# Optimization experiments

Hardware: AMD Instinct MI355X
Metric: run time of the kernel (lower is better)

## Reference

```python
import jax, jax.numpy as jnp
import numpy as np

N = 10000        # num nodes
E = 160000       # num edges
C = 128          # hidden_channels
SCALE = 0.0625   # scale_factor = 1/avg_degree
EPS = 1.1920929e-07  # torch RMSNorm default eps = finfo(float32).eps


def setup_inputs() -> dict:
    key = jax.random.key(0)
    ks = jax.random.split(key, 10)
    s = jax.random.normal(ks[0], (N, 1, C), dtype=jnp.float32)
    v = jax.random.normal(ks[1], (N, 3, C), dtype=jnp.float32)
    edge_index = jax.random.randint(ks[2], (2, E), 0, N, dtype=jnp.int64)
    rbf_filter = jax.random.normal(ks[3], (E, 1, 3 * C), dtype=jnp.float32)
    edge_vector = jax.random.normal(ks[4], (E, 3), dtype=jnp.float32)
    # phi MLP params (Linear(C,C) -> SiLU -> Dropout(eval) -> Linear(C,3C))
    w1 = jax.random.normal(ks[5], (C, C), dtype=jnp.float32) / np.sqrt(C)
    b1 = jnp.zeros((C,), dtype=jnp.float32)
    w2 = jax.random.normal(ks[6], (3 * C, C), dtype=jnp.float32) / np.sqrt(C)
    b2 = jnp.zeros((3 * C,), dtype=jnp.float32)
    rms_w = jnp.ones((C,), dtype=jnp.float32)  # RMSNorm elementwise affine weight
    return {"s": s, "v": v, "edge_index": edge_index, "rbf_filter": rbf_filter,
            "edge_vector": edge_vector, "w1": w1, "b1": b1, "w2": w2, "b2": b2,
            "rms_w": rms_w}


def reference(s, v, edge_index, rbf_filter, edge_vector, w1, b1, w2, b2, rms_w):
    i, j = edge_index[0], edge_index[1]
    # RMSNorm over last dim
    s_norm = s * jax.lax.rsqrt(jnp.mean(s * s, axis=-1, keepdims=True) + EPS) * rms_w
    # phi MLP (dropout is identity in eval mode)
    h = jax.nn.silu(jnp.einsum('nkc,dc->nkd', s_norm, w1) + b1)
    phi_s = jnp.einsum('nkc,dc->nkd', h, w2) + b2          # [N,1,3C]
    filt = phi_s[j] * rbf_filter                           # [E,1,3C]
    m_s, m_vv, m_vs = jnp.split(filt, 3, axis=-1)          # each [E,1,C]
    ds = jax.ops.segment_sum(m_s, i, num_segments=N)       # [N,1,C]
    gate = v[j] * m_vv + edge_vector[:, :, None] * m_vs    # [E,3,C]
    dv = jax.ops.segment_sum(gate, i, num_segments=N)      # [N,3,C]
    s_out = s + ds * SCALE
    v_out = v + dv * SCALE
    return s_out, v_out
```

## Files before the change

### kernel.cpp

```cpp
#include <hip/hip_runtime.h>
#include <hip/hip_fp16.h>
#include <math.h>

#define NN 10000
#define NE 160000
#define CH 128
#define SCALE_F 0.0625f
#define EPS_F 1.1920929e-07f

__device__ __forceinline__ unsigned short f2bf(float x) {
    unsigned int u = __float_as_uint(x);
    u += 0x7FFFu + ((u >> 16) & 1u);
    return (unsigned short)(u >> 16);
}
__device__ __forceinline__ unsigned int pack2bf(float a, float b) {
    return (unsigned int)f2bf(a) | ((unsigned int)f2bf(b) << 16);
}
__device__ __forceinline__ float bf_lo(unsigned int u) { return __uint_as_float(u << 16); }
__device__ __forceinline__ float bf_hi(unsigned int u) { return __uint_as_float(u & 0xFFFF0000u); }
__device__ __forceinline__ float4 bfq(uint2 u) {
    return make_float4(bf_lo(u.x), bf_hi(u.x), bf_lo(u.y), bf_hi(u.y));
}

__global__ __launch_bounds__(256) void detect_zero_kernel(const int* __restrict__ ei,
                                                          int* __restrict__ flag,
                                                          int* __restrict__ counts) {
    int t = blockIdx.x * 256 + threadIdx.x;
    if (t < NN) counts[t] = 0;
    if (blockIdx.x == 0 && threadIdx.x < 64) {
        int val = ei[2 * threadIdx.x + 1];
        unsigned long long b = __ballot(val != 0);
        if (threadIdx.x == 0) *flag = (b == 0ULL) ? 1 : 0;
    }
}

__global__ __launch_bounds__(256) void transpose_w_kernel(const float* __restrict__ w1,
                                                          const float* __restrict__ w2,
                                                          float* __restrict__ w1t,
                                                          float* __restrict__ w2t) {
    int idx = blockIdx.x * 256 + threadIdx.x;
    if (idx < 128 * 128) {
        int c = idx >> 7, d = idx & 127;
        w1t[c * 128 + d] = w1[d * 128 + c];
    } else {
        int o = idx - 128 * 128;
        int c = o / 384, d = o - c * 384;
        w2t[c * 384 + d] = w2[d * 128 + c];
    }
}

__global__ __launch_bounds__(256) void count_kernel(const int* __restrict__ ei,
                                                    const int* __restrict__ flag,
                                                    int* __restrict__ counts) {
    int e = blockIdx.x * 256 + threadIdx.x;
    if (e >= NE) return;
    int i = (*flag) ? ei[2 * (size_t)e] : ei[e];
    atomicAdd(&counts[i], 1);
}

__global__ __launch_bounds__(1024) void scan_kernel(const int* __restrict__ counts,
                                                    int* __restrict__ offsets,
                                                    int* __restrict__ cursor) {
    __shared__ int sm[1024];
    const int t = threadIdx.x;
    const int base = t * 10;
    int vals[10];
    int lsum = 0;
    #pragma unroll
    for (int k = 0; k < 10; ++k) {
        int idx = base + k;
        int v = (idx < NN) ? counts[idx] : 0;
        vals[k] = v;
        lsum += v;
    }
    sm[t] = lsum;
    __syncthreads();
    #pragma unroll
    for (int off = 1; off < 1024; off <<= 1) {
        int add = (t >= off) ? sm[t - off] : 0;
        __syncthreads();
        sm[t] += add;
        __syncthreads();
    }
    int run = sm[t] - lsum;
    #pragma unroll
    for (int k = 0; k < 10; ++k) {
        int idx = base + k;
        if (idx < NN) { offsets[idx] = run; cursor[idx] = run; }
        run += vals[k];
    }
}

__global__ __launch_bounds__(256) void bucket_kernel(const int* __restrict__ ei,
                                                     const int* __restrict__ flag,
                                                     const float* __restrict__ ev,
                                                     int* __restrict__ cursor,
                                                     int4* __restrict__ bucket) {
    int e = blockIdx.x * 256 + threadIdx.x;
    if (e >= NE) return;
    int i, j;
    if (*flag) {
        i = ei[2 * (size_t)e];
        j = ei[2 * ((size_t)NE + e)];
    } else {
        i = ei[e];
        j = ei[NE + e];
    }
    float e0 = ev[(size_t)e * 3 + 0];
    float e1 = ev[(size_t)e * 3 + 1];
    float e2 = ev[(size_t)e * 3 + 2];
    __half2 h01 = __floats2half2_rn(e0, e1);
    __half  h2v = __float2half_rn(e2);
    unsigned int u01 = *reinterpret_cast<unsigned int*>(&h01);
    unsigned int u2  = (unsigned int)(*reinterpret_cast<unsigned short*>(&h2v));
    int pos = atomicAdd(&cursor[i], 1);
    bucket[pos] = make_int4(e, j, (int)u01, (int)u2);
}

__global__ __launch_bounds__(128) void phi_kernel(const float* __restrict__ s,
                                                  const float* __restrict__ v,
                                                  const float* __restrict__ w1t,
                                                  const float* __restrict__ b1,
                                                  const float* __restrict__ w2t,
                                                  const float* __restrict__ b2,
                                                  const float* __restrict__ rms_w,
                                                  unsigned int* __restrict__ rec) {
    __shared__ float xw[2][8][128];
    __shared__ float hh[2][8][128];

    const int t = threadIdx.x;
    const int wv = t >> 6;
    const int l = t & 63;
    const int half = l >> 5;
    const int q = l & 31;
    const int nbase = blockIdx.x * 16 + wv * 8;

    #pragma unroll
    for (int n = 0; n < 8; ++n) {
        const int gn = nbase + n;
        const float2* vsrc = (const float2*)(v + (size_t)gn * 384);
        unsigned int* vdst = rec + (size_t)gn * 384 + 192;
        #pragma unroll
        for (int k = 0; k < 3; ++k) {
            float2 a = vsrc[k * 64 + l];
            vdst[k * 64 + l] = pack2bf(a.x, a.y);
        }
    }

    {
        const float4 rw = ((const float4*)rms_w)[q];
        #pragma unroll
        for (int r = 0; r < 4; ++r) {
            const int n = half * 4 + r;
            const int gn = nbase + n;
            float4 sv = ((const float4*)(s + (size_t)gn * CH))[q];
            float ss = sv.x * sv.x + sv.y * sv.y + sv.z * sv.z + sv.w * sv.w;
            #pragma unroll
            for (int off = 16; off > 0; off >>= 1) ss += __shfl_xor(ss, off, 32);
            const float sc = rsqrtf(ss * (1.0f / CH) + EPS_F);
            float4 o;
            o.x = sv.x * sc * rw.x;
            o.y = sv.y * sc * rw.y;
            o.z = sv.z * sc * rw.z;
            o.w = sv.w * sc * rw.w;
            *(float4*)&xw[wv][n][q * 4] = o;
        }
    }
    __syncthreads();

    {
        float4 acc[8];
        const float4 bia = ((const float4*)b1)[q];
        #pragma unroll
        for (int n = 0; n < 8; ++n)
            acc[n] = (half == 0) ? bia : make_float4(0.f, 0.f, 0.f, 0.f);

        #pragma unroll 4
        for (int it = 0; it < 64; ++it) {
            const int c = 2 * it + half;
            const float4 w = *(const float4*)(w1t + (size_t)c * 128 + 4 * q);
            #pragma unroll
            for (int n = 0; n < 8; ++n) {
                const float xv = xw[wv][n][c];
                acc[n].x = fmaf(xv, w.x, acc[n].x);
                acc[n].y = fmaf(xv, w.y, acc[n].y);
                acc[n].z = fmaf(xv, w.z, acc[n].z);
                acc[n].w = fmaf(xv, w.w, acc[n].w);
            }
        }
        #pragma unroll
        for (int n = 0; n < 8; ++n) {
            acc[n].x += __shfl_xor(acc[n].x, 32);
            acc[n].y += __shfl_xor(acc[n].y, 32);
            acc[n].z += __shfl_xor(acc[n].z, 32);
            acc[n].w += __shfl_xor(acc[n].w, 32);
        }
        #pragma unroll
        for (int r = 0; r < 4; ++r) {
            const int n = half * 4 + r;
            float4 a = acc[n];
            a.x = a.x / (1.0f + __expf(-a.x));
            a.y = a.y / (1.0f + __expf(-a.y));
            a.z = a.z / (1.0f + __expf(-a.z));
            a.w = a.w / (1.0f + __expf(-a.w));
            *(float4*)&hh[wv][n][q * 4] = a;
        }
    }
    __syncthreads();

    #pragma unroll 1
    for (int sg = 0; sg < 3; ++sg) {
        float4 acc[8];
        const float4 bia = ((const float4*)(b2 + 128 * sg))[q];
        #pragma unroll
        for (int n = 0; n < 8; ++n)
            acc[n] = (half == 0) ? bia : make_float4(0.f, 0.f, 0.f, 0.f);

        #pragma unroll 4
        for (int it = 0; it < 64; ++it) {
            const int c = 2 * it + half;
            const float4 w = *(const float4*)(w2t + (size_t)c * 384 + 128 * sg + 4 * q);
            #pragma unroll
            for (int n = 0; n < 8; ++n) {
                const float hv = hh[wv][n][c];
                acc[n].x = fmaf(hv, w.x, acc[n].x);
                acc[n].y = fmaf(hv, w.y, acc[n].y);
                acc[n].z = fmaf(hv, w.z, acc[n].z);
                acc[n].w = fmaf(hv, w.w, acc[n].w);
            }
        }
        #pragma unroll
        for (int n = 0; n < 8; ++n) {
            acc[n].x += __shfl_xor(acc[n].x, 32);
            acc[n].y += __shfl_xor(acc[n].y, 32);
            acc[n].z += __shfl_xor(acc[n].z, 32);
            acc[n].w += __shfl_xor(acc[n].w, 32);
        }
        #pragma unroll
        for (int r = 0; r < 4; ++r) {
            const int n = half * 4 + r;
            uint2 pk;
            pk.x = pack2bf(acc[n].x, acc[n].y);
            pk.y = pack2bf(acc[n].z, acc[n].w);
            *(uint2*)(rec + (size_t)(nbase + n) * 384 + 64 * sg + 2 * q) = pk;
        }
    }
}

__global__ __launch_bounds__(256) void gather_kernel(const float* __restrict__ s,
                                                     const float* __restrict__ v,
                                                     const unsigned int* __restrict__ rec,
                                                     const float* __restrict__ rbf,
                                                     const int* __restrict__ offsets,
                                                     const int* __restrict__ counts,
                                                     const int4* __restrict__ bucket,
                                                     float* __restrict__ out_s,
                                                     float* __restrict__ out_v) {
    const int t = threadIdx.x;
    const int n = blockIdx.x * 4 + (t >> 6);
    const int l = t & 63;
    const int half = l >> 5;
    const int q = l & 31;

    float4 acc_s = make_float4(0.f, 0.f, 0.f, 0.f);
    float4 av0 = acc_s, av1 = acc_s, av2 = acc_s;

    const int beg = offsets[n];
    const int deg = counts[n];
    const int npair = deg >> 1;
    const int4* bk = bucket + beg;

    int4 ent = make_int4(0, 0, 0, 0);
    if (npair > 0) ent = bk[half];

    for (int p = 0; p < npair; ++p) {
        int4 entn = ent;
        if (p + 1 < npair) entn = bk[2 * (p + 1) + half];

        const unsigned int* rj = rec + (size_t)ent.y * 384;
        const float*        rb = rbf + (size_t)ent.x * 384;

        uint2 uS  = ((const uint2*)(rj +   0))[q];
        uint2 uVV = ((const uint2*)(rj +  64))[q];
        uint2 uVS = ((const uint2*)(rj + 128))[q];
        uint2 uV0 = ((const uint2*)(rj + 192))[q];
        uint2 uV1 = ((const uint2*)(rj + 256))[q];
        uint2 uV2 = ((const uint2*)(rj + 320))[q];
        float4 rS  = ((const float4*)(rb +   0))[q];
        float4 rVV = ((const float4*)(rb + 128))[q];
        float4 rVS = ((const float4*)(rb + 256))[q];

        __half2 h01 = *reinterpret_cast<const __half2*>(&ent.z);
        float2 ev01 = __half22float2(h01);
        unsigned short h2u = (unsigned short)(ent.w & 0xFFFF);
        float ev2 = __half2float(*reinterpret_cast<const __half*>(&h2u));

        float4 ps = bfq(uS);
        acc_s.x = fmaf(ps.x, rS.x, acc_s.x);
        acc_s.y = fmaf(ps.y, rS.y, acc_s.y);
        acc_s.z = fmaf(ps.z, rS.z, acc_s.z);
        acc_s.w = fmaf(ps.w, rS.w, acc_s.w);

        float4 pv = bfq(uVV);
        float4 pw = bfq(uVS);
        float4 mvv = make_float4(pv.x * rVV.x, pv.y * rVV.y, pv.z * rVV.z, pv.w * rVV.w);
        float4 mvs = make_float4(pw.x * rVS.x, pw.y * rVS.y, pw.z * rVS.z, pw.w * rVS.w);

        float4 v0 = bfq(uV0), v1 = bfq(uV1), v2 = bfq(uV2);
        av0.x = fmaf(v0.x, mvv.x, fmaf(ev01.x, mvs.x, av0.x));
        av0.y = fmaf(v0.y, mvv.y, fmaf(ev01.x, mvs.y, av0.y));
        av0.z = fmaf(v0.z, mvv.z, fmaf(ev01.x, mvs.z, av0.z));
        av0.w = fmaf(v0.w, mvv.w, fmaf(ev01.x, mvs.w, av0.w));
        av1.x = fmaf(v1.x, mvv.x, fmaf(ev01.y, mvs.x, av1.x));
        av1.y = fmaf(v1.y, mvv.y, fmaf(ev01.y, mvs.y, av1.y));
        av1.z = fmaf(v1.z, mvv.z, fmaf(ev01.y, mvs.z, av1.z));
        av1.w = fmaf(v1.w, mvv.w, fmaf(ev01.y, mvs.w, av1.w));
        av2.x = fmaf(v2.x, mvv.x, fmaf(ev2, mvs.x, av2.x));
        av2.y = fmaf(v2.y, mvv.y, fmaf(ev2, mvs.y, av2.y));
        av2.z = fmaf(v2.z, mvv.z, fmaf(ev2, mvs.z, av2.z));
        av2.w = fmaf(v2.w, mvv.w, fmaf(ev2, mvs.w, av2.w));

        ent = entn;
    }

    if ((deg & 1) && half == 0) {
        int4 te = bk[deg - 1];
        const unsigned int* rj = rec + (size_t)te.y * 384;
        const float*        rb = rbf + (size_t)te.x * 384;

        uint2 uS  = ((const uint2*)(rj +   0))[q];
        uint2 uVV = ((const uint2*)(rj +  64))[q];
        uint2 uVS = ((const uint2*)(rj + 128))[q];
        uint2 uV0 = ((const uint2*)(rj + 192))[q];
        uint2 uV1 = ((const uint2*)(rj + 256))[q];
        uint2 uV2 = ((const uint2*)(rj + 320))[q];
        float4 rS  = ((const float4*)(rb +   0))[q];
        float4 rVV = ((const float4*)(rb + 128))[q];
        float4 rVS = ((const float4*)(rb + 256))[q];

        __half2 h01 = *reinterpret_cast<const __half2*>(&te.z);
        float2 ev01 = __half22float2(h01);
        unsigned short h2u = (unsigned short)(te.w & 0xFFFF);
        float ev2 = __half2float(*reinterpret_cast<const __half*>(&h2u));

        float4 ps = bfq(uS);
        acc_s.x = fmaf(ps.x, rS.x, acc_s.x);
        acc_s.y = fmaf(ps.y, rS.y, acc_s.y);
        acc_s.z = fmaf(ps.z, rS.z, acc_s.z);
        acc_s.w = fmaf(ps.w, rS.w, acc_s.w);

        float4 pv = bfq(uVV);
        float4 pw = bfq(uVS);
        float4 mvv = make_float4(pv.x * rVV.x, pv.y * rVV.y, pv.z * rVV.z, pv.w * rVV.w);
        float4 mvs = make_float4(pw.x * rVS.x, pw.y * rVS.y, pw.z * rVS.z, pw.w * rVS.w);

        float4 v0 = bfq(uV0), v1 = bfq(uV1), v2 = bfq(uV2);
        av0.x = fmaf(v0.x, mvv.x, fmaf(ev01.x, mvs.x, av0.x));
        av0.y = fmaf(v0.y, mvv.y, fmaf(ev01.x, mvs.y, av0.y));
        av0.z = fmaf(v0.z, mvv.z, fmaf(ev01.x, mvs.z, av0.z));
        av0.w = fmaf(v0.w, mvv.w, fmaf(ev01.x, mvs.w, av0.w));
        av1.x = fmaf(v1.x, mvv.x, fmaf(ev01.y, mvs.x, av1.x));
        av1.y = fmaf(v1.y, mvv.y, fmaf(ev01.y, mvs.y, av1.y));
        av1.z = fmaf(v1.z, mvv.z, fmaf(ev01.y, mvs.z, av1.z));
        av1.w = fmaf(v1.w, mvv.w, fmaf(ev01.y, mvs.w, av1.w));
        av2.x = fmaf(v2.x, mvv.x, fmaf(ev2, mvs.x, av2.x));
        av2.y = fmaf(v2.y, mvv.y, fmaf(ev2, mvs.y, av2.y));
        av2.z = fmaf(v2.z, mvv.z, fmaf(ev2, mvs.z, av2.z));
        av2.w = fmaf(v2.w, mvv.w, fmaf(ev2, mvs.w, av2.w));
    }

    acc_s.x += __shfl_xor(acc_s.x, 32);
    acc_s.y += __shfl_xor(acc_s.y, 32);
    acc_s.z += __shfl_xor(acc_s.z, 32);
    acc_s.w += __shfl_xor(acc_s.w, 32);
    av0.x += __shfl_xor(av0.x, 32);
    av0.y += __shfl_xor(av0.y, 32);
    av0.z += __shfl_xor(av0.z, 32);
    av0.w += __shfl_xor(av0.w, 32);
    av1.x += __shfl_xor(av1.x, 32);
    av1.y += __shfl_xor(av1.y, 32);
    av1.z += __shfl_xor(av1.z, 32);
    av1.w += __shfl_xor(av1.w, 32);
    av2.x += __shfl_xor(av2.x, 32);
    av2.y += __shfl_xor(av2.y, 32);
    av2.z += __shfl_xor(av2.z, 32);
    av2.w += __shfl_xor(av2.w, 32);

    const size_t nb = (size_t)n;
    if (half == 0) {
        float4 sv = ((const float4*)(s + nb * CH))[q];
        ((float4*)(out_s + nb * CH))[q] =
            make_float4(sv.x + SCALE_F * acc_s.x, sv.y + SCALE_F * acc_s.y,
                        sv.z + SCALE_F * acc_s.z, sv.w + SCALE_F * acc_s.w);
        float4 w0 = ((const float4*)(v + nb * 384))[q];
        ((float4*)(out_v + nb * 384))[q] =
            make_float4(w0.x + SCALE_F * av0.x, w0.y + SCALE_F * av0.y,
                        w0.z + SCALE_F * av0.z, w0.w + SCALE_F * av0.w);
    } else {
        float4 w1 = ((const float4*)(v + nb * 384 + 128))[q];
        ((float4*)(out_v + nb * 384 + 128))[q] =
            make_float4(w1.x + SCALE_F * av1.x, w1.y + SCALE_F * av1.y,
                        w1.z + SCALE_F * av1.z, w1.w + SCALE_F * av1.w);
        float4 w2 = ((const float4*)(v + nb * 384 + 256))[q];
        ((float4*)(out_v + nb * 384 + 256))[q] =
            make_float4(w2.x + SCALE_F * av2.x, w2.y + SCALE_F * av2.y,
                        w2.z + SCALE_F * av2.z, w2.w + SCALE_F * av2.w);
    }
}

extern "C" void kernel_launch(void* const* d_in, const int* in_sizes, int n_in,
                              void* d_out, int out_size, void* d_ws, size_t ws_size,
                              hipStream_t stream) {
    const float* s    = (const float*)d_in[0];
    const float* v    = (const float*)d_in[1];
    const int*   ei   = (const int*)d_in[2];
    const float* rbf  = (const float*)d_in[3];
    const float* ev   = (const float*)d_in[4];
    const float* w1   = (const float*)d_in[5];
    const float* b1   = (const float*)d_in[6];
    const float* w2   = (const float*)d_in[7];
    const float* b2   = (const float*)d_in[8];
    const float* rmsw = (const float*)d_in[9];

    float* out   = (float*)d_out;
    float* out_s = out;
    float* out_v = out + (size_t)NN * CH;

    char* ws = (char*)d_ws;
    unsigned int* rec = (unsigned int*)ws;     ws += (size_t)NN * 384 * sizeof(unsigned int);
    int* i64flag = (int*)ws;                   ws += 64;
    int* counts  = (int*)ws;                   ws += (size_t)NN * sizeof(int);
    int* offsets = (int*)ws;                   ws += (size_t)NN * sizeof(int);
    int* cursor  = (int*)ws;                   ws += (size_t)NN * sizeof(int) + 48;
    int4* bucket = (int4*)ws;                  ws += (size_t)NE * sizeof(int4);
    float* w1t   = (float*)ws;                 ws += (size_t)128 * 128 * sizeof(float);
    float* w2t   = (float*)ws;

    detect_zero_kernel<<<(NN + 255) / 256, 256, 0, stream>>>(ei, i64flag, counts);
    transpose_w_kernel<<<256, 256, 0, stream>>>(w1, w2, w1t, w2t);
    count_kernel<<<(NE + 255) / 256, 256, 0, stream>>>(ei, i64flag, counts);
    scan_kernel<<<1, 1024, 0, stream>>>(counts, offsets, cursor);
    bucket_kernel<<<(NE + 255) / 256, 256, 0, stream>>>(ei, i64flag, ev, cursor, bucket);
    phi_kernel<<<NN / 16, 128, 0, stream>>>(s, v, w1t, b1, w2t, b2, rmsw, rec);
    gather_kernel<<<NN / 4, 256, 0, stream>>>(s, v, rec, rbf, offsets, counts, bucket,
                                              out_s, out_v);
}
```

Measured before the change: 463.1 us.

## Interleave per-node record layout and software-pipeline gather loads two edges ahead

```diff
diff --git a/kernel.cpp b/kernel.cpp
--- a/kernel.cpp
+++ b/kernel.cpp
@@ -18,8 +18,11 @@
 }
 __device__ __forceinline__ float bf_lo(unsigned int u) { return __uint_as_float(u << 16); }
 __device__ __forceinline__ float bf_hi(unsigned int u) { return __uint_as_float(u & 0xFFFF0000u); }
-__device__ __forceinline__ float4 bfq(uint2 u) {
-    return make_float4(bf_lo(u.x), bf_hi(u.x), bf_lo(u.y), bf_hi(u.y));
+
+typedef float f4v __attribute__((ext_vector_type(4)));
+__device__ __forceinline__ float4 ntload4(const float* p) {
+    f4v t = __builtin_nontemporal_load((const f4v*)p);
+    return make_float4(t.x, t.y, t.z, t.w);
 }
 
 __global__ __launch_bounds__(256) void detect_zero_kernel(const int* __restrict__ ei,
@@ -135,15 +138,19 @@
     const int q = l & 31;
     const int nbase = blockIdx.x * 16 + wv * 8;
 
-    #pragma unroll
-    for (int n = 0; n < 8; ++n) {
-        const int gn = nbase + n;
-        const float2* vsrc = (const float2*)(v + (size_t)gn * 384);
-        unsigned int* vdst = rec + (size_t)gn * 384 + 192;
-        #pragma unroll
-        for (int k = 0; k < 3; ++k) {
-            float2 a = vsrc[k * 64 + l];
-            vdst[k * 64 + l] = pack2bf(a.x, a.y);
+    {
+        const int cg = l >> 1;
+        const int u  = l & 1;
+        #pragma unroll
+        for (int nn = 0; nn < 8; ++nn) {
+            const int gn = nbase + nn;
+            const float2* vsrc = (const float2*)(v + (size_t)gn * 384);
+            unsigned int* vdst = rec + (size_t)gn * 384 + cg * 12 + 6 + u;
+            #pragma unroll
+            for (int k = 0; k < 3; ++k) {
+                float2 a = vsrc[k * 64 + l];
+                vdst[2 * k] = pack2bf(a.x, a.y);
+            }
         }
     }
 
@@ -242,9 +249,64 @@
             uint2 pk;
             pk.x = pack2bf(acc[n].x, acc[n].y);
             pk.y = pack2bf(acc[n].z, acc[n].w);
-            *(uint2*)(rec + (size_t)(nbase + n) * 384 + 64 * sg + 2 * q) = pk;
-        }
-    }
+            *(uint2*)(rec + (size_t)(nbase + n) * 384 + q * 12 + 2 * sg) = pk;
+        }
+    }
+}
+
+struct EdgeRegs {
+    uint4 u0, u1, u2;
+    float4 f0, f1, f2;
+};
+
+__device__ __forceinline__ void issue_loads(const unsigned int* __restrict__ rec,
+                                            const float* __restrict__ rbf,
+                                            int4 ent, int q, EdgeRegs& R) {
+    const uint4* rj = (const uint4*)(rec + (size_t)ent.y * 384) + 3 * q;
+    R.u0 = rj[0];
+    R.u1 = rj[1];
+    R.u2 = rj[2];
+    const float* rb = rbf + (size_t)ent.x * 384;
+    R.f0 = ntload4(rb + 4 * q);
+    R.f1 = ntload4(rb + 128 + 4 * q);
+    R.f2 = ntload4(rb + 256 + 4 * q);
+}
+
+__device__ __forceinline__ void edge_accum(int4 ent, const EdgeRegs& R,
+                                           float4& acc_s, float4& av0,
+                                           float4& av1, float4& av2) {
+    __half2 h01 = *reinterpret_cast<const __half2*>(&ent.z);
+    float2 ev01 = __half22float2(h01);
+    unsigned short h2u = (unsigned short)(ent.w & 0xFFFF);
+    float ev2 = __half2float(*reinterpret_cast<const __half*>(&h2u));
+
+    float4 ps = make_float4(bf_lo(R.u0.x), bf_hi(R.u0.x), bf_lo(R.u0.y), bf_hi(R.u0.y));
+    acc_s.x = fmaf(ps.x, R.f0.x, acc_s.x);
+    acc_s.y = fmaf(ps.y, R.f0.y, acc_s.y);
+    acc_s.z = fmaf(ps.z, R.f0.z, acc_s.z);
+    acc_s.w = fmaf(ps.w, R.f0.w, acc_s.w);
+
+    float4 pv = make_float4(bf_lo(R.u0.z), bf_hi(R.u0.z), bf_lo(R.u0.w), bf_hi(R.u0.w));
+    float4 pw = make_float4(bf_lo(R.u1.x), bf_hi(R.u1.x), bf_lo(R.u1.y), bf_hi(R.u1.y));
+    float4 mvv = make_float4(pv.x * R.f1.x, pv.y * R.f1.y, pv.z * R.f1.z, pv.w * R.f1.w);
+    float4 mvs = make_float4(pw.x * R.f2.x, pw.y * R.f2.y, pw.z * R.f2.z, pw.w * R.f2.w);
+
+    float4 v0 = make_float4(bf_lo(R.u1.z), bf_hi(R.u1.z), bf_lo(R.u1.w), bf_hi(R.u1.w));
+    float4 v1 = make_float4(bf_lo(R.u2.x), bf_hi(R.u2.x), bf_lo(R.u2.y), bf_hi(R.u2.y));
+    float4 v2 = make_float4(bf_lo(R.u2.z), bf_hi(R.u2.z), bf_lo(R.u2.w), bf_hi(R.u2.w));
+
+    av0.x = fmaf(v0.x, mvv.x, fmaf(ev01.x, mvs.x, av0.x));
+    av0.y = fmaf(v0.y, mvv.y, fmaf(ev01.x, mvs.y, av0.y));
+    av0.z = fmaf(v0.z, mvv.z, fmaf(ev01.x, mvs.z, av0.z));
+    av0.w = fmaf(v0.w, mvv.w, fmaf(ev01.x, mvs.w, av0.w));
+    av1.x = fmaf(v1.x, mvv.x, fmaf(ev01.y, mvs.x, av1.x));
+    av1.y = fmaf(v1.y, mvv.y, fmaf(ev01.y, mvs.y, av1.y));
+    av1.z = fmaf(v1.z, mvv.z, fmaf(ev01.y, mvs.z, av1.z));
+    av1.w = fmaf(v1.w, mvv.w, fmaf(ev01.y, mvs.w, av1.w));
+    av2.x = fmaf(v2.x, mvv.x, fmaf(ev2, mvs.x, av2.x));
+    av2.y = fmaf(v2.y, mvv.y, fmaf(ev2, mvs.y, av2.y));
+    av2.z = fmaf(v2.z, mvv.z, fmaf(ev2, mvs.z, av2.z));
+    av2.w = fmaf(v2.w, mvv.w, fmaf(ev2, mvs.w, av2.w));
 }
 
 __global__ __launch_bounds__(256) void gather_kernel(const float* __restrict__ s,
@@ -270,103 +332,27 @@
     const int npair = deg >> 1;
     const int4* bk = bucket + beg;
 
-    int4 ent = make_int4(0, 0, 0, 0);
-    if (npair > 0) ent = bk[half];
-
+    int4 eA = make_int4(0, 0, 0, 0), eB = eA, eC = eA;
+    EdgeRegs RA, RB;
+    if (npair > 0) eA = bk[half];
+    if (npair > 1) eB = bk[2 + half];
+    if (npair > 0) issue_loads(rec, rbf, eA, q, RA);
+    if (npair > 1) issue_loads(rec, rbf, eB, q, RB);
+    if (npair > 2) eC = bk[4 + half];
+
+    #pragma unroll 2
     for (int p = 0; p < npair; ++p) {
-        int4 entn = ent;
-        if (p + 1 < npair) entn = bk[2 * (p + 1) + half];
-
-        const unsigned int* rj = rec + (size_t)ent.y * 384;
-        const float*        rb = rbf + (size_t)ent.x * 384;
-
-        uint2 uS  = ((const uint2*)(rj +   0))[q];
-        uint2 uVV = ((const uint2*)(rj +  64))[q];
-        uint2 uVS = ((const uint2*)(rj + 128))[q];
-        uint2 uV0 = ((const uint2*)(rj + 192))[q];
-        uint2 uV1 = ((const uint2*)(rj + 256))[q];
-        uint2 uV2 = ((const uint2*)(rj + 320))[q];
-        float4 rS  = ((const float4*)(rb +   0))[q];
-        float4 rVV = ((const float4*)(rb + 128))[q];
-        float4 rVS = ((const float4*)(rb + 256))[q];
-
-        __half2 h01 = *reinterpret_cast<const __half2*>(&ent.z);
-        float2 ev01 = __half22float2(h01);
-        unsigned short h2u = (unsigned short)(ent.w & 0xFFFF);
-        float ev2 = __half2float(*reinterpret_cast<const __half*>(&h2u));
-
-        float4 ps = bfq(uS);
-        acc_s.x = fmaf(ps.x, rS.x, acc_s.x);
-        acc_s.y = fmaf(ps.y, rS.y, acc_s.y);
-        acc_s.z = fmaf(ps.z, rS.z, acc_s.z);
-        acc_s.w = fmaf(ps.w, rS.w, acc_s.w);
-
-        float4 pv = bfq(uVV);
-        float4 pw = bfq(uVS);
-        float4 mvv = make_float4(pv.x * rVV.x, pv.y * rVV.y, pv.z * rVV.z, pv.w * rVV.w);
-        float4 mvs = make_float4(pw.x * rVS.x, pw.y * rVS.y, pw.z * rVS.z, pw.w * rVS.w);
-
-        float4 v0 = bfq(uV0), v1 = bfq(uV1), v2 = bfq(uV2);
-        av0.x = fmaf(v0.x, mvv.x, fmaf(ev01.x, mvs.x, av0.x));
-        av0.y = fmaf(v0.y, mvv.y, fmaf(ev01.x, mvs.y, av0.y));
-        av0.z = fmaf(v0.z, mvv.z, fmaf(ev01.x, mvs.z, av0.z));
-        av0.w = fmaf(v0.w, mvv.w, fmaf(ev01.x, mvs.w, av0.w));
-        av1.x = fmaf(v1.x, mvv.x, fmaf(ev01.y, mvs.x, av1.x));
-        av1.y = fmaf(v1.y, mvv.y, fmaf(ev01.y, mvs.y, av1.y));
-        av1.z = fmaf(v1.z, mvv.z, fmaf(ev01.y, mvs.z, av1.z));
-        av1.w = fmaf(v1.w, mvv.w, fmaf(ev01.y, mvs.w, av1.w));
-        av2.x = fmaf(v2.x, mvv.x, fmaf(ev2, mvs.x, av2.x));
-        av2.y = fmaf(v2.y, mvv.y, fmaf(ev2, mvs.y, av2.y));
-        av2.z = fmaf(v2.z, mvv.z, fmaf(ev2, mvs.z, av2.z));
-        av2.w = fmaf(v2.w, mvv.w, fmaf(ev2, mvs.w, av2.w));
-
-        ent = entn;
+        edge_accum(eA, RA, acc_s, av0, av1, av2);
+        eA = eB; RA = RB; eB = eC;
+        if (p + 2 < npair) issue_loads(rec, rbf, eB, q, RB);
+        if (p + 3 < npair) eC = bk[2 * (p + 3) + half];
     }
 
     if ((deg & 1) && half == 0) {
         int4 te = bk[deg - 1];
-        const unsigned int* rj = rec + (size_t)te.y * 384;
-        const float*        rb = rbf + (size_t)te.x * 384;
-
-        uint2 uS  = ((const uint2*)(rj +   0))[q];
-        uint2 uVV = ((const uint2*)(rj +  64))[q];
-        uint2 uVS = ((const uint2*)(rj + 128))[q];
-        uint2 uV0 = ((const uint2*)(rj + 192))[q];
-        uint2 uV1 = ((const uint2*)(rj + 256))[q];
-        uint2 uV2 = ((const uint2*)(rj + 320))[q];
-        float4 rS  = ((const float4*)(rb +   0))[q];
-        float4 rVV = ((const float4*)(rb + 128))[q];
-        float4 rVS = ((const float4*)(rb + 256))[q];
-
-        __half2 h01 = *reinterpret_cast<const __half2*>(&te.z);
-        float2 ev01 = __half22float2(h01);
-        unsigned short h2u = (unsigned short)(te.w & 0xFFFF);
-        float ev2 = __half2float(*reinterpret_cast<const __half*>(&h2u));
-
-        float4 ps = bfq(uS);
-        acc_s.x = fmaf(ps.x, rS.x, acc_s.x);
-        acc_s.y = fmaf(ps.y, rS.y, acc_s.y);
-        acc_s.z = fmaf(ps.z, rS.z, acc_s.z);
-        acc_s.w = fmaf(ps.w, rS.w, acc_s.w);
-
-        float4 pv = bfq(uVV);
-        float4 pw = bfq(uVS);
-        float4 mvv = make_float4(pv.x * rVV.x, pv.y * rVV.y, pv.z * rVV.z, pv.w * rVV.w);
-        float4 mvs = make_float4(pw.x * rVS.x, pw.y * rVS.y, pw.z * rVS.z, pw.w * rVS.w);
-
-        float4 v0 = bfq(uV0), v1 = bfq(uV1), v2 = bfq(uV2);
-        av0.x = fmaf(v0.x, mvv.x, fmaf(ev01.x, mvs.x, av0.x));
-        av0.y = fmaf(v0.y, mvv.y, fmaf(ev01.x, mvs.y, av0.y));
-        av0.z = fmaf(v0.z, mvv.z, fmaf(ev01.x, mvs.z, av0.z));
-        av0.w = fmaf(v0.w, mvv.w, fmaf(ev01.x, mvs.w, av0.w));
-        av1.x = fmaf(v1.x, mvv.x, fmaf(ev01.y, mvs.x, av1.x));
-        av1.y = fmaf(v1.y, mvv.y, fmaf(ev01.y, mvs.y, av1.y));
-        av1.z = fmaf(v1.z, mvv.z, fmaf(ev01.y, mvs.z, av1.z));
-        av1.w = fmaf(v1.w, mvv.w, fmaf(ev01.y, mvs.w, av1.w));
-        av2.x = fmaf(v2.x, mvv.x, fmaf(ev2, mvs.x, av2.x));
-        av2.y = fmaf(v2.y, mvv.y, fmaf(ev2, mvs.y, av2.y));
-        av2.z = fmaf(v2.z, mvv.z, fmaf(ev2, mvs.z, av2.z));
-        av2.w = fmaf(v2.w, mvv.w, fmaf(ev2, mvs.w, av2.w));
+        EdgeRegs RT;
+        issue_loads(rec, rbf, te, q, RT);
+        edge_accum(te, RT, acc_s, av0, av1, av2);
     }
 
     acc_s.x += __shfl_xor(acc_s.x, 32);
```

After: 462.6 us. No clear change (-0.1%).
